# Kernel tuning notes

Measured on AMD Instinct MI355X. Metric: run time of the kernel, lower is better.

Reference implementation:

```python
import jax, jax.numpy as jnp
import numpy as np

N_NODES = 100000
N_EDGES = 3200000
HID = 52
N_LAYERS = 3


def setup_inputs() -> dict:
    key = jax.random.key(0)
    ks = jax.random.split(key, 6)
    x = jax.random.normal(ks[0], (N_NODES, HID), dtype=jnp.float32)
    edge_index = jax.random.randint(ks[1], (2, N_EDGES), 0, N_NODES, dtype=jnp.int32)
    w1 = jax.random.normal(ks[2], (N_LAYERS, HID, 2 * HID), dtype=jnp.float32) * 0.1
    b1 = jnp.zeros((N_LAYERS, 2 * HID), dtype=jnp.float32)
    w2 = jax.random.normal(ks[3], (N_LAYERS, 2 * HID, HID), dtype=jnp.float32) * 0.1
    b2 = jnp.zeros((N_LAYERS, HID), dtype=jnp.float32)
    eps = jnp.zeros((N_LAYERS,), dtype=jnp.float32)
    lin_w = jax.random.normal(ks[4], (HID * (N_LAYERS + 1), HID), dtype=jnp.float32) * 0.1
    lin_b = jnp.zeros((HID,), dtype=jnp.float32)
    return {"x": x, "edge_index": edge_index, "w1": w1, "b1": b1,
            "w2": w2, "b2": b2, "eps": eps, "lin_w": lin_w, "lin_b": lin_b}


def reference(x, edge_index, w1, b1, w2, b2, eps, lin_w, lin_b):
    src, dst = edge_index[0], edge_index[1]
    n = x.shape[0]
    h = x
    h_list = [x]
    for l in range(N_LAYERS):
        # GINConv: sum-aggregate neighbor features at target nodes
        agg = jax.ops.segment_sum(h[src], dst, num_segments=n)  # [N, HID]
        z = (1.0 + eps[l]) * h + agg
        # 2-layer MLP: Linear -> ReLU -> Linear
        z = jnp.maximum(z @ w1[l] + b1[l], 0.0) @ w2[l] + b2[l]
        # outer ReLU (dropout p=0 is identity)
        h = jnp.maximum(z, 0.0)
        h_list.append(h)
    node_repr = jnp.concatenate(h_list, axis=1)  # [N, HID*(L+1)]
    return node_repr @ lin_w + lin_b
```

## Files before the change

### kernel.cpp

```cpp
#include <hip/hip_runtime.h>

#define HID 52
#define HID2 104
#define P1_CHUNK 8192
#define NBIN_MAX 512

typedef unsigned short ushort_t;
typedef unsigned int uint_t;
typedef short bf16x8 __attribute__((ext_vector_type(8)));
typedef float f32x4 __attribute__((ext_vector_type(4)));
typedef float f32x2 __attribute__((ext_vector_type(2)));

__device__ __forceinline__ ushort_t f2bf(float f) {
    union { float f; uint_t u; } c; c.f = f;
    uint_t u = c.u + 0x7FFFu + ((c.u >> 16) & 1u);
    return (ushort_t)(u >> 16);
}
__device__ __forceinline__ float bflo(uint_t u) {
    union { uint_t u; float f; } c; c.u = u << 16; return c.f;
}
__device__ __forceinline__ float bfhi(uint_t u) {
    union { uint_t u; float f; } c; c.u = u & 0xFFFF0000u; return c.f;
}
__device__ __forceinline__ f32x2 unpk(uint_t u) {
    return (f32x2){bflo(u), bfhi(u)};
}


__global__ __launch_bounds__(256) void bhist_kernel(const int* __restrict__ dst,
                                                    int* __restrict__ ghist, int E) {
    __shared__ int lh[NBIN_MAX];
    int tid = threadIdx.x;
    lh[tid] = 0; lh[tid + 256] = 0;
    __syncthreads();
    int base = blockIdx.x * P1_CHUNK;
    int cend = min(P1_CHUNK, E - base);
    for (int i = tid; i < cend; i += 256) atomicAdd(&lh[dst[base + i] >> 8], 1);
    __syncthreads();
    int c = lh[tid];       if (c) atomicAdd(&ghist[tid], c);
    c = lh[tid + 256];     if (c) atomicAdd(&ghist[tid + 256], c);
}

__global__ __launch_bounds__(256) void bscan_kernel(const int* __restrict__ ghist,
                                                    int* __restrict__ binstart,
                                                    int* __restrict__ gcur,
                                                    int NBIN, int E) {
    __shared__ int c[NBIN_MAX];
    __shared__ int ps[256];
    int tid = threadIdx.x;
    int b0 = 2 * tid, b1 = 2 * tid + 1;
    c[b0] = ghist[b0]; c[b1] = ghist[b1];
    __syncthreads();
    int pair = c[b0] + c[b1];
    ps[tid] = pair;
    __syncthreads();
    for (int off = 1; off < 256; off <<= 1) {
        int t = (tid >= off) ? ps[tid - off] : 0;
        __syncthreads();
        ps[tid] += t;
        __syncthreads();
    }
    int ex = ps[tid] - pair;
    binstart[b0] = ex;        gcur[b0] = ex;
    binstart[b1] = ex + c[b0]; gcur[b1] = ex + c[b0];
    if (tid == 0) binstart[NBIN] = E;
}

__global__ __launch_bounds__(256) void pass1_kernel(const int* __restrict__ src,
                                                    const int* __restrict__ dst,
                                                    int* __restrict__ gcur,
                                                    uint_t* __restrict__ packed, int E) {
    __shared__ uint_t stage[P1_CHUNK];
    __shared__ ushort_t sbin[P1_CHUNK];
    __shared__ int cnt[NBIN_MAX];
    __shared__ int sst[NBIN_MAX];
    __shared__ int curs[NBIN_MAX];
    __shared__ int gbase[NBIN_MAX];
    __shared__ int ps[256];
    int tid = threadIdx.x;
    int base = blockIdx.x * P1_CHUNK;
    int cend = min(P1_CHUNK, E - base);
    cnt[tid] = 0; cnt[tid + 256] = 0;
    __syncthreads();
    for (int i = tid; i < cend; i += 256) atomicAdd(&cnt[dst[base + i] >> 8], 1);
    __syncthreads();
    int b0 = 2 * tid, b1 = 2 * tid + 1;
    int c0 = cnt[b0], c1 = cnt[b1];
    int pair = c0 + c1;
    ps[tid] = pair;
    __syncthreads();
    for (int off = 1; off < 256; off <<= 1) {
        int t = (tid >= off) ? ps[tid - off] : 0;
        __syncthreads();
        ps[tid] += t;
        __syncthreads();
    }
    int ex = ps[tid] - pair;
    sst[b0] = ex;       curs[b0] = ex;
    sst[b1] = ex + c0;  curs[b1] = ex + c0;
    gbase[b0] = c0 ? atomicAdd(&gcur[b0], c0) : 0;
    gbase[b1] = c1 ? atomicAdd(&gcur[b1], c1) : 0;
    __syncthreads();
    for (int i = tid; i < cend; i += 256) {
        int d = dst[base + i];
        int s = src[base + i];
        int b = d >> 8;
        int pos = atomicAdd(&curs[b], 1);
        stage[pos] = ((uint_t)s << 8) | (uint_t)(d & 255);
        sbin[pos] = (ushort_t)b;
    }
    __syncthreads();
    for (int i = tid; i < cend; i += 256) {
        int b = sbin[i];
        packed[gbase[b] + (i - sst[b])] = stage[i];
    }
}

__global__ __launch_bounds__(256) void pass2_kernel(const uint_t* __restrict__ packed,
                                                    const int* __restrict__ binstart,
                                                    int* __restrict__ srcsorted,
                                                    int* __restrict__ nrs,
                                                    int* __restrict__ ndeg, int N) {
    __shared__ int ncnt[256];
    __shared__ int ps[256];
    __shared__ int curs[256];
    int b = blockIdx.x;
    int beg = binstart[b], end = binstart[b + 1];
    int obase = beg + b * 4096;
    int tid = threadIdx.x;
    ncnt[tid] = 0;
    __syncthreads();
    for (int i = beg + tid; i < end; i += 256) atomicAdd(&ncnt[packed[i] & 255u], 1);
    __syncthreads();
    int v = ncnt[tid];
    int pv = (v + 15) & ~15;
    ps[tid] = pv;
    __syncthreads();
    for (int off = 1; off < 256; off <<= 1) {
        int t = (tid >= off) ? ps[tid - off] : 0;
        __syncthreads();
        ps[tid] += t;
        __syncthreads();
    }
    int start = obase + ps[tid] - pv;
    int node = b * 256 + tid;
    if (node < N) { nrs[node] = start; ndeg[node] = pv; }
    curs[tid] = start;
    __syncthreads();
    for (int i = beg + tid; i < end; i += 256) {
        uint_t p = packed[i];
        int pos = atomicAdd(&curs[p & 255u], 1);
        srcsorted[pos] = (int)(p >> 8);
    }
    __syncthreads();
    for (int i = start + v; i < start + pv; i++) srcsorted[i] = N;
}


__global__ void conv_x_kernel(const float* __restrict__ x, ushort_t* __restrict__ xb, int n) {
    int t = blockIdx.x * 256 + threadIdx.x;
    if (t >= n * 16) return;
    int node = t >> 4, p = t & 15;
    int c0 = p * 4;
    ushort_t o[4];
#pragma unroll
    for (int j = 0; j < 4; j++) {
        int c = c0 + j;
        o[j] = (c < HID) ? f2bf(x[(size_t)node * HID + c]) : 0;
    }
    uint_t u0 = (uint_t)o[0] | ((uint_t)o[1] << 16);
    uint_t u1 = (uint_t)o[2] | ((uint_t)o[3] << 16);
    *(uint2*)(xb + (size_t)node * 64 + c0) = make_uint2(u0, u1);
}

__global__ void zero_pad_rows_kernel(ushort_t* xb, ushort_t* h1b, ushort_t* h2b,
                                     ushort_t* h3b, int N) {
    int t = threadIdx.x;
    ushort_t* arr = (t < 64) ? xb : (t < 128) ? h1b : (t < 192) ? h2b : h3b;
    arr[(size_t)N * 64 + (t & 63)] = 0;
}

__global__ void conv_w_kernel(const float* __restrict__ w1, const float* __restrict__ w2,
                              const float* __restrict__ lin_w,
                              ushort_t* __restrict__ w1f, ushort_t* __restrict__ w2f,
                              ushort_t* __restrict__ linf) {
    int t = blockIdx.x * 256 + threadIdx.x;
    int gid = t >> 6, lane = t & 63;
    if (gid >= 122) return;
    int m = lane & 15, q = lane >> 4;
    ushort_t o[8];
    ushort_t* dstp;
    if (gid < 42) {
        int l = gid / 14, r = gid % 14, ct = r >> 1, ks = r & 1;
        int nn = ct * 16 + m;
#pragma unroll
        for (int j = 0; j < 8; j++) {
            int k = ks * 32 + q * 8 + j;
            o[j] = (k < HID && nn < HID2) ? f2bf(w1[((size_t)l * HID + k) * HID2 + nn]) : 0;
        }
        dstp = w1f + ((size_t)(l * 14 + ct * 2 + ks) * 64 + lane) * 8;
    } else if (gid < 90) {
        int g2 = gid - 42, l = g2 / 16, r = g2 % 16, ct = r >> 2, ks = r & 3;
        int nn = ct * 16 + m;
#pragma unroll
        for (int j = 0; j < 8; j++) {
            int k = ks * 32 + q * 8 + j;
            o[j] = (k < HID2 && nn < HID) ? f2bf(w2[((size_t)l * HID2 + k) * HID + nn]) : 0;
        }
        dstp = w2f + ((size_t)(l * 16 + ct * 4 + ks) * 64 + lane) * 8;
    } else {
        int g2 = gid - 90, ct = g2 >> 3, ks = g2 & 7;
        int nn = ct * 16 + m;
#pragma unroll
        for (int j = 0; j < 8; j++) {
            int kg = ks * 32 + q * 8 + j;
            int seg = kg >> 6, kk = kg & 63;
            o[j] = (kk < HID && nn < HID) ? f2bf(lin_w[((size_t)seg * HID + kk) * HID + nn]) : 0;
        }
        dstp = linf + ((size_t)(ct * 8 + ks) * 64 + lane) * 8;
    }
    uint4 u;
    u.x = (uint_t)o[0] | ((uint_t)o[1] << 16);
    u.y = (uint_t)o[2] | ((uint_t)o[3] << 16);
    u.z = (uint_t)o[4] | ((uint_t)o[5] << 16);
    u.w = (uint_t)o[6] | ((uint_t)o[7] << 16);
    *(uint4*)dstp = u;
}

__global__ __launch_bounds__(256) void agg_kernel(const ushort_t* __restrict__ hb,
                                                  const int* __restrict__ nrs,
                                                  const int* __restrict__ ndeg,
                                                  const int* __restrict__ srcsorted,
                                                  const float* __restrict__ eps,
                                                  ushort_t* __restrict__ zb, int n) {
    int wid = (blockIdx.x * blockDim.x + threadIdx.x) >> 6;
    if (wid >= n) return;
    int lane = threadIdx.x & 63;
    int g = lane >> 3, sub = lane & 7;
    int beg = nrs[wid];
    int total = ndeg[wid];
    const ushort_t* hsub = hb + sub * 8;

    f32x2 A0 = {0,0}, A1 = {0,0}, A2 = {0,0}, A3 = {0,0};
    f32x2 B0 = {0,0}, B1 = {0,0}, B2 = {0,0}, B3 = {0,0};
    for (int b = 0; b < total; b += 64) {
        int cnt = min(64, total - b);
        int idx = (lane < cnt) ? srcsorted[beg + b + lane] : 0;
        int jmax = cnt >> 3;
        for (int j = 0; j < jmax; j += 2) {
            int s0 = __shfl(idx, (j << 3) | g);
            int s1 = __shfl(idx, ((j + 1) << 3) | g);
            uint4 v0 = *(const uint4*)(hsub + (size_t)s0 * 64);
            uint4 v1 = *(const uint4*)(hsub + (size_t)s1 * 64);
            A0 += unpk(v0.x); A1 += unpk(v0.y); A2 += unpk(v0.z); A3 += unpk(v0.w);
            B0 += unpk(v1.x); B1 += unpk(v1.y); B2 += unpk(v1.z); B3 += unpk(v1.w);
        }
    }
    A0 += B0; A1 += B1; A2 += B2; A3 += B3;
    float a0 = A0.x, a1 = A0.y, a2 = A1.x, a3 = A1.y;
    float a4 = A2.x, a5 = A2.y, a6 = A3.x, a7 = A3.y;
#pragma unroll
    for (int msk = 8; msk <= 32; msk <<= 1) {
        a0 += __shfl_xor(a0, msk); a1 += __shfl_xor(a1, msk);
        a2 += __shfl_xor(a2, msk); a3 += __shfl_xor(a3, msk);
        a4 += __shfl_xor(a4, msk); a5 += __shfl_xor(a5, msk);
        a6 += __shfl_xor(a6, msk); a7 += __shfl_xor(a7, msk);
    }
    if (lane < 8) {
        float sc = 1.0f + eps[0];
        uint4 sv = *(const uint4*)(hb + (size_t)wid * 64 + lane * 8);
        float o0 = fmaf(sc, bflo(sv.x), a0), o1 = fmaf(sc, bfhi(sv.x), a1);
        float o2 = fmaf(sc, bflo(sv.y), a2), o3 = fmaf(sc, bfhi(sv.y), a3);
        float o4 = fmaf(sc, bflo(sv.z), a4), o5 = fmaf(sc, bfhi(sv.z), a5);
        float o6 = fmaf(sc, bflo(sv.w), a6), o7 = fmaf(sc, bfhi(sv.w), a7);
        uint4 u;
        u.x = (uint_t)f2bf(o0) | ((uint_t)f2bf(o1) << 16);
        u.y = (uint_t)f2bf(o2) | ((uint_t)f2bf(o3) << 16);
        u.z = (uint_t)f2bf(o4) | ((uint_t)f2bf(o5) << 16);
        u.w = (uint_t)f2bf(o6) | ((uint_t)f2bf(o7) << 16);
        *(uint4*)(zb + (size_t)wid * 64 + lane * 8) = u;
    }
}

#define HSTRIDE 136
__global__ __launch_bounds__(256) void mlp_kernel(const ushort_t* __restrict__ zb,
                                                  const ushort_t* __restrict__ w1f,
                                                  const float* __restrict__ b1,
                                                  const ushort_t* __restrict__ w2f,
                                                  const float* __restrict__ b2,
                                                  ushort_t* __restrict__ hbout, int n) {
    __shared__ ushort_t hid[64 * HSTRIDE];
    int tid = threadIdx.x;
    int w = tid >> 6, lane = tid & 63, m = lane & 15, q = lane >> 4;
    for (int i = tid; i < 64 * 32; i += 256) {
        int r = i >> 5, c = HID2 + (i & 31);
        hid[r * HSTRIDE + c] = 0;
    }
    __syncthreads();

    int nb = blockIdx.x * 64 + w * 16;
    f32x4 acc1[7];
#pragma unroll
    for (int ct = 0; ct < 7; ct++) {
        int col = ct * 16 + m;
        float bv = (col < HID2) ? b1[col] : 0.f;
        acc1[ct] = (f32x4){bv, bv, bv, bv};
    }
    int anode = min(nb + m, n - 1);
#pragma unroll
    for (int ks = 0; ks < 2; ks++) {
        bf16x8 a = *(const bf16x8*)(zb + (size_t)anode * 64 + ks * 32 + q * 8);
#pragma unroll
        for (int ct = 0; ct < 7; ct++) {
            bf16x8 b = *(const bf16x8*)(w1f + ((size_t)(ct * 2 + ks) * 64 + lane) * 8);
            acc1[ct] = __builtin_amdgcn_mfma_f32_16x16x32_bf16(a, b, acc1[ct], 0, 0, 0);
        }
    }
#pragma unroll
    for (int ct = 0; ct < 7; ct++) {
#pragma unroll
        for (int r = 0; r < 4; r++) {
            float v = fmaxf(acc1[ct][r], 0.f);
            int row = w * 16 + q * 4 + r;
            hid[row * HSTRIDE + ct * 16 + m] = f2bf(v);
        }
    }
    f32x4 acc2[4];
#pragma unroll
    for (int ct = 0; ct < 4; ct++) {
        int col = ct * 16 + m;
        float bv = (col < HID) ? b2[col] : 0.f;
        acc2[ct] = (f32x4){bv, bv, bv, bv};
    }
#pragma unroll
    for (int ks = 0; ks < 4; ks++) {
        bf16x8 a = *(const bf16x8*)&hid[(w * 16 + m) * HSTRIDE + ks * 32 + q * 8];
#pragma unroll
        for (int ct = 0; ct < 4; ct++) {
            bf16x8 b = *(const bf16x8*)(w2f + ((size_t)(ct * 4 + ks) * 64 + lane) * 8);
            acc2[ct] = __builtin_amdgcn_mfma_f32_16x16x32_bf16(a, b, acc2[ct], 0, 0, 0);
        }
    }
#pragma unroll
    for (int ct = 0; ct < 4; ct++) {
#pragma unroll
        for (int r = 0; r < 4; r++) {
            int node = nb + q * 4 + r;
            if (node < n) {
                float v = fmaxf(acc2[ct][r], 0.f);
                hbout[(size_t)node * 64 + ct * 16 + m] = f2bf(v);
            }
        }
    }
}

__global__ __launch_bounds__(256) void final_kernel(const ushort_t* __restrict__ xb,
                                                    const ushort_t* __restrict__ h1b,
                                                    const ushort_t* __restrict__ h2b,
                                                    const ushort_t* __restrict__ h3b,
                                                    const ushort_t* __restrict__ linf,
                                                    const float* __restrict__ lin_b,
                                                    float* __restrict__ out, int ntiles) {
    int tid = threadIdx.x;
    int w = tid >> 6, lane = tid & 63, m = lane & 15, q = lane >> 4;
    int tile = blockIdx.x * 4 + w;
    if (tile >= ntiles) return;
    int nb = tile * 16;
    const ushort_t* segs[4] = {xb, h1b, h2b, h3b};
    f32x4 acc[4];
#pragma unroll
    for (int ct = 0; ct < 4; ct++) {
        int col = ct * 16 + m;
        float bv = (col < HID) ? lin_b[col] : 0.f;
        acc[ct] = (f32x4){bv, bv, bv, bv};
    }
#pragma unroll
    for (int ks = 0; ks < 8; ks++) {
        const ushort_t* p = segs[ks >> 1];
        bf16x8 a = *(const bf16x8*)(p + (size_t)(nb + m) * 64 + (ks & 1) * 32 + q * 8);
#pragma unroll
        for (int ct = 0; ct < 4; ct++) {
            bf16x8 b = *(const bf16x8*)(linf + ((size_t)(ct * 8 + ks) * 64 + lane) * 8);
            acc[ct] = __builtin_amdgcn_mfma_f32_16x16x32_bf16(a, b, acc[ct], 0, 0, 0);
        }
    }
#pragma unroll
    for (int ct = 0; ct < 4; ct++) {
        int col = ct * 16 + m;
        if (col < HID) {
#pragma unroll
            for (int r = 0; r < 4; r++)
                out[(size_t)(nb + q * 4 + r) * HID + col] = acc[ct][r];
        }
    }
}

extern "C" void kernel_launch(void* const* d_in, const int* in_sizes, int n_in,
                              void* d_out, int out_size, void* d_ws, size_t ws_size,
                              hipStream_t stream) {
    const float* x     = (const float*)d_in[0];
    const int*   ei    = (const int*)d_in[1];
    const float* w1    = (const float*)d_in[2];
    const float* b1    = (const float*)d_in[3];
    const float* w2    = (const float*)d_in[4];
    const float* b2    = (const float*)d_in[5];
    const float* eps   = (const float*)d_in[6];
    const float* lin_w = (const float*)d_in[7];
    const float* lin_b = (const float*)d_in[8];
    float* out = (float*)d_out;

    const int N = in_sizes[0] / HID;
    const int E = in_sizes[1] / 2;
    const int* src = ei;
    const int* dst = ei + E;

    const int NBIN = (N + 255) / 256;

    char* p = (char*)d_ws;
    const size_t ROWS = (size_t)(N + 1) * 64 * 2;
    ushort_t* xb  = (ushort_t*)p;  p += ROWS;
    ushort_t* zb  = (ushort_t*)p;  p += ROWS;
    ushort_t* h1b = (ushort_t*)p;  p += ROWS;
    ushort_t* h2b = (ushort_t*)p;  p += ROWS;
    ushort_t* h3b = (ushort_t*)p;  p += ROWS;
    ushort_t* w1f = (ushort_t*)p;  p += 3 * 14 * 512 * 2;
    ushort_t* w2f = (ushort_t*)p;  p += 3 * 16 * 512 * 2;
    ushort_t* linf= (ushort_t*)p;  p += 32 * 512 * 2;
    int* ghist    = (int*)p;       p += 528 * 4;
    int* binstart = (int*)p;       p += 528 * 4;
    int* gcur     = (int*)p;       p += 528 * 4;
    int* nrs      = (int*)p;       p += (size_t)(N + 4) * 4;
    int* ndeg     = (int*)p;       p += (size_t)(N + 4) * 4;
    uint_t* packed = (uint_t*)p;   p += (size_t)E * 4;
    int* srcsorted = (int*)p;

    ushort_t* hbs[4] = {xb, h1b, h2b, h3b};

    const int BLK = 256;
    const int NP1 = (E + P1_CHUNK - 1) / P1_CHUNK;
    dim3 blk(BLK);
    dim3 grid_agg(((size_t)N * 64 + BLK - 1) / BLK);

    hipMemsetAsync(ghist, 0, 512 * sizeof(int), stream);
    bhist_kernel<<<NP1, blk, 0, stream>>>(dst, ghist, E);
    bscan_kernel<<<1, blk, 0, stream>>>(ghist, binstart, gcur, NBIN, E);
    pass1_kernel<<<NP1, blk, 0, stream>>>(src, dst, gcur, packed, E);
    pass2_kernel<<<NBIN, blk, 0, stream>>>(packed, binstart, srcsorted, nrs, ndeg, N);
    conv_x_kernel<<<(N * 16 + BLK - 1) / BLK, blk, 0, stream>>>(x, xb, N);
    zero_pad_rows_kernel<<<1, 256, 0, stream>>>(xb, h1b, h2b, h3b, N);
    conv_w_kernel<<<(122 * 64 + BLK - 1) / BLK, blk, 0, stream>>>(w1, w2, lin_w, w1f, w2f, linf);

    const int NBUCK = (N + 63) / 64;
    for (int l = 0; l < 3; l++) {
        agg_kernel<<<grid_agg, blk, 0, stream>>>(hbs[l], nrs, ndeg, srcsorted, eps + l, zb, N);
        mlp_kernel<<<NBUCK, blk, 0, stream>>>(zb,
                                              w1f + (size_t)l * 14 * 512,
                                              b1 + (size_t)l * HID2,
                                              w2f + (size_t)l * 16 * 512,
                                              b2 + (size_t)l * HID,
                                              hbs[l + 1], N);
    }
    final_kernel<<<(6250 + 3) / 4 + 1, blk, 0, stream>>>(xb, h1b, h2b, h3b, linf, lin_b,
                                                         out, (N + 15) / 16);
}
```

Measured before the change: 410.4 us.

## Merge setup kernels into one launch and software-pipeline neighbor index loads in aggregation

Folds the memset, x conversion, pad-row zeroing and weight conversion into a single setup kernel, removing several launches. The aggregation loop now prefetches the next batch of source indices directly from memory, not via a per-64 load plus shuffles. It also processes four neighbor rows per iteration to raise memory-level parallelism. The prefetch reads past the node's segment, relying on padding in srcsorted; out-of-range slots are masked to the zero pad row N.

```diff
diff --git a/kernel.cpp b/kernel.cpp
--- a/kernel.cpp
+++ b/kernel.cpp
@@ -156,36 +156,45 @@
     for (int i = start + v; i < start + pv; i++) srcsorted[i] = N;
 }
 
-
-__global__ void conv_x_kernel(const float* __restrict__ x, ushort_t* __restrict__ xb, int n) {
-    int t = blockIdx.x * 256 + threadIdx.x;
-    if (t >= n * 16) return;
-    int node = t >> 4, p = t & 15;
-    int c0 = p * 4;
-    ushort_t o[4];
-#pragma unroll
-    for (int j = 0; j < 4; j++) {
-        int c = c0 + j;
-        o[j] = (c < HID) ? f2bf(x[(size_t)node * HID + c]) : 0;
-    }
-    uint_t u0 = (uint_t)o[0] | ((uint_t)o[1] << 16);
-    uint_t u1 = (uint_t)o[2] | ((uint_t)o[3] << 16);
-    *(uint2*)(xb + (size_t)node * 64 + c0) = make_uint2(u0, u1);
-}
-
-__global__ void zero_pad_rows_kernel(ushort_t* xb, ushort_t* h1b, ushort_t* h2b,
-                                     ushort_t* h3b, int N) {
-    int t = threadIdx.x;
-    ushort_t* arr = (t < 64) ? xb : (t < 128) ? h1b : (t < 192) ? h2b : h3b;
-    arr[(size_t)N * 64 + (t & 63)] = 0;
-}
-
-__global__ void conv_w_kernel(const float* __restrict__ w1, const float* __restrict__ w2,
-                              const float* __restrict__ lin_w,
-                              ushort_t* __restrict__ w1f, ushort_t* __restrict__ w2f,
-                              ushort_t* __restrict__ linf) {
-    int t = blockIdx.x * 256 + threadIdx.x;
-    int gid = t >> 6, lane = t & 63;
+__global__ __launch_bounds__(256) void setup_kernel(const float* __restrict__ x,
+                                                    const float* __restrict__ w1,
+                                                    const float* __restrict__ w2,
+                                                    const float* __restrict__ lin_w,
+                                                    ushort_t* __restrict__ xb,
+                                                    ushort_t* __restrict__ h1b,
+                                                    ushort_t* __restrict__ h2b,
+                                                    ushort_t* __restrict__ h3b,
+                                                    ushort_t* __restrict__ w1f,
+                                                    ushort_t* __restrict__ w2f,
+                                                    ushort_t* __restrict__ linf,
+                                                    int* __restrict__ ghist,
+                                                    int n, int nxblk) {
+    int blk = blockIdx.x;
+    int tid = threadIdx.x;
+    if (blk < nxblk) {
+        int t = blk * 256 + tid;
+        if (t >= n * 16) return;
+        int node = t >> 4, pp = t & 15;
+        int c0 = pp * 4;
+        ushort_t o[4];
+#pragma unroll
+        for (int j = 0; j < 4; j++) {
+            int c = c0 + j;
+            o[j] = (c < HID) ? f2bf(x[(size_t)node * HID + c]) : 0;
+        }
+        uint_t u0 = (uint_t)o[0] | ((uint_t)o[1] << 16);
+        uint_t u1 = (uint_t)o[2] | ((uint_t)o[3] << 16);
+        *(uint2*)(xb + (size_t)node * 64 + c0) = make_uint2(u0, u1);
+        return;
+    }
+    if (blk == nxblk) {
+        ushort_t* arr = (tid < 64) ? xb : (tid < 128) ? h1b : (tid < 192) ? h2b : h3b;
+        arr[(size_t)n * 64 + (tid & 63)] = 0;
+        ghist[tid] = 0; ghist[tid + 256] = 0;
+        return;
+    }
+    int gid = (blk - nxblk - 1) * 4 + (tid >> 6);
+    int lane = tid & 63;
     if (gid >= 122) return;
     int m = lane & 15, q = lane >> 4;
     ushort_t o[8];
@@ -240,20 +249,26 @@
     int beg = nrs[wid];
     int total = ndeg[wid];
     const ushort_t* hsub = hb + sub * 8;
+    const int* ss = srcsorted + beg + g;
 
     f32x2 A0 = {0,0}, A1 = {0,0}, A2 = {0,0}, A3 = {0,0};
     f32x2 B0 = {0,0}, B1 = {0,0}, B2 = {0,0}, B3 = {0,0};
-    for (int b = 0; b < total; b += 64) {
-        int cnt = min(64, total - b);
-        int idx = (lane < cnt) ? srcsorted[beg + b + lane] : 0;
-        int jmax = cnt >> 3;
-        for (int j = 0; j < jmax; j += 2) {
-            int s0 = __shfl(idx, (j << 3) | g);
-            int s1 = __shfl(idx, ((j + 1) << 3) | g);
-            uint4 v0 = *(const uint4*)(hsub + (size_t)s0 * 64);
-            uint4 v1 = *(const uint4*)(hsub + (size_t)s1 * 64);
+    if (total > 0) {
+        int f0 = ss[0], f1 = ss[8], f2r = ss[16], f3r = ss[24];
+        for (int b = 0; b < total; b += 32) {
+            bool ok = (b + 16) < total;
+            int e0 = f0, e1 = f1;
+            int e2 = ok ? f2r : n;
+            int e3 = ok ? f3r : n;
+            f0 = ss[b + 32]; f1 = ss[b + 40]; f2r = ss[b + 48]; f3r = ss[b + 56];
+            uint4 v0 = *(const uint4*)(hsub + (size_t)e0 * 64);
+            uint4 v1 = *(const uint4*)(hsub + (size_t)e1 * 64);
+            uint4 v2 = *(const uint4*)(hsub + (size_t)e2 * 64);
+            uint4 v3 = *(const uint4*)(hsub + (size_t)e3 * 64);
             A0 += unpk(v0.x); A1 += unpk(v0.y); A2 += unpk(v0.z); A3 += unpk(v0.w);
             B0 += unpk(v1.x); B1 += unpk(v1.y); B2 += unpk(v1.z); B3 += unpk(v1.w);
+            A0 += unpk(v2.x); A1 += unpk(v2.y); A2 += unpk(v2.z); A3 += unpk(v2.w);
+            B0 += unpk(v3.x); B1 += unpk(v3.y); B2 += unpk(v3.z); B3 += unpk(v3.w);
         }
     }
     A0 += B0; A1 += B1; A2 += B2; A3 += B3;
@@ -438,17 +453,17 @@
 
     const int BLK = 256;
     const int NP1 = (E + P1_CHUNK - 1) / P1_CHUNK;
+    const int NXBLK = (N * 16 + BLK - 1) / BLK;
     dim3 blk(BLK);
     dim3 grid_agg(((size_t)N * 64 + BLK - 1) / BLK);
 
-    hipMemsetAsync(ghist, 0, 512 * sizeof(int), stream);
+    setup_kernel<<<NXBLK + 1 + 31, blk, 0, stream>>>(x, w1, w2, lin_w,
+                                                     xb, h1b, h2b, h3b,
+                                                     w1f, w2f, linf, ghist, N, NXBLK);
     bhist_kernel<<<NP1, blk, 0, stream>>>(dst, ghist, E);
     bscan_kernel<<<1, blk, 0, stream>>>(ghist, binstart, gcur, NBIN, E);
     pass1_kernel<<<NP1, blk, 0, stream>>>(src, dst, gcur, packed, E);
     pass2_kernel<<<NBIN, blk, 0, stream>>>(packed, binstart, srcsorted, nrs, ndeg, N);
-    conv_x_kernel<<<(N * 16 + BLK - 1) / BLK, blk, 0, stream>>>(x, xb, N);
-    zero_pad_rows_kernel<<<1, 256, 0, stream>>>(xb, h1b, h2b, h3b, N);
-    conv_w_kernel<<<(122 * 64 + BLK - 1) / BLK, blk, 0, stream>>>(w1, w2, lin_w, w1f, w2f, linf);
 
     const int NBUCK = (N + 63) / 64;
     for (int l = 0; l < 3; l++) {
```

Result: no change. 403.8 us (-1.6%).
